# Performance work log

Hardware: AMD Instinct MI355X
Metric: run time of the kernel (lower is better)

## Reference

```python
import jax, jax.numpy as jnp
import numpy as np

N_NODES = 100000
N_HEDGES = 200000
E = 1200000
N_GRAPHS = 512
H = 64            # h_dim
HE = 35           # hedge_fea_dim (CHGConv default)
HOUT = 128        # hout_dim
L = 3             # n_layers
EPS = 1e-5


def _segment_mean(vals, seg, num):
    s = jax.ops.segment_sum(vals, seg, num_segments=num)
    cnt = jax.ops.segment_sum(jnp.ones((vals.shape[0], 1), vals.dtype), seg, num_segments=num)
    return s / jnp.maximum(cnt, 1.0)


def _bn(v, g, b):
    # BatchNorm1d in training mode: batch mean / biased variance
    m = jnp.mean(v, axis=0)
    var = jnp.var(v, axis=0)
    return g * (v - m) * jax.lax.rsqrt(var + EPS) + b


def _chg_conv(x, node_idx, hedge_idx, hattr,
              Wf1, bf1, Wc1, bc1, Wf2, bf2, Wc2, bc2,
              gf, btf, gc, btc, go, bto):
    # gather node feats into hedges, mean-aggregate per hyperedge
    agg = _segment_mean(x[node_idx], hedge_idx, N_HEDGES)          # [NH, H]
    msg = jnp.concatenate([agg, hattr], axis=1)                    # [NH, H+HE]
    z_f = _bn(msg @ Wf1 + bf1, gf, btf)
    z_c = _bn(msg @ Wc1 + bc1, gc, btc)
    hedge_feats = jax.nn.sigmoid(z_f) * jax.nn.softplus(z_c)       # [NH, HE]
    z = jnp.concatenate([x[node_idx], hedge_feats[hedge_idx]], axis=-1)  # [E, H+HE]
    out = jax.nn.sigmoid(z @ Wf2 + bf2) * jax.nn.softplus(z @ Wc2 + bc2)  # [E, H]
    out = _segment_mean(out, node_idx, N_NODES)                    # [N, H]
    out = _bn(out, go, bto)
    return jax.nn.softplus(out + x)


def setup_inputs() -> dict:
    key = jax.random.key(0)
    ks = jax.random.split(key, 32)
    x = jax.random.normal(ks[0], (N_NODES, 92), dtype=jnp.float32)
    node_idx = jax.random.randint(ks[1], (E,), 0, N_NODES)
    hedge_idx = jax.random.randint(ks[2], (E,), 0, N_HEDGES)
    hyperedge_index = jnp.stack([node_idx, hedge_idx], axis=0)     # [2, E]
    hedge_attr = jax.random.normal(ks[3], (N_HEDGES, HE), dtype=jnp.float32)
    batch = jnp.sort(jax.random.randint(ks[4], (N_NODES,), 0, N_GRAPHS))

    s = 0.05
    d = H + HE
    inp = {
        'x': x, 'hyperedge_index': hyperedge_index, 'hedge_attr': hedge_attr, 'batch': batch,
        'We': jax.random.normal(ks[5], (92, H)) * s, 'be': jnp.zeros((H,)),
        'Wf1': jax.random.normal(ks[6], (L, d, HE)) * s, 'bf1': jnp.zeros((L, HE)),
        'Wc1': jax.random.normal(ks[7], (L, d, HE)) * s, 'bc1': jnp.zeros((L, HE)),
        'Wf2': jax.random.normal(ks[8], (L, d, H)) * s, 'bf2': jnp.zeros((L, H)),
        'Wc2': jax.random.normal(ks[9], (L, d, H)) * s, 'bc2': jnp.zeros((L, H)),
        'bn_f_g': jnp.ones((L, HE)), 'bn_f_b': jnp.zeros((L, HE)),
        'bn_c_g': jnp.ones((L, HE)), 'bn_c_b': jnp.zeros((L, HE)),
        'bn_o_g': jnp.ones((L, H)), 'bn_o_b': jnp.zeros((L, H)),
        'Wl2': jax.random.normal(ks[10], (H, HOUT)) * s, 'bl2': jnp.zeros((HOUT,)),
        'Wo': jax.random.normal(ks[11], (HOUT, 1)) * s, 'bo': jnp.zeros((1,)),
    }
    return inp


def reference(x, hyperedge_index, hedge_attr, batch, We, be,
              Wf1, bf1, Wc1, bc1, Wf2, bf2, Wc2, bc2,
              bn_f_g, bn_f_b, bn_c_g, bn_c_b, bn_o_g, bn_o_b,
              Wl2, bl2, Wo, bo):
    node_idx = hyperedge_index[0]
    hedge_idx = hyperedge_index[1]
    h = x @ We + be                                                # embed 92 -> H
    for i in range(L):                                             # only mconvs are used in forward
        h = _chg_conv(h, node_idx, hedge_idx, hedge_attr,
                      Wf1[i], bf1[i], Wc1[i], bc1[i], Wf2[i], bf2[i], Wc2[i], bc2[i],
                      bn_f_g[i], bn_f_b[i], bn_c_g[i], bn_c_b[i], bn_o_g[i], bn_o_b[i])
        h = jax.nn.relu(h)
    g = _segment_mean(h, batch, N_GRAPHS)                          # [G, H]
    g = jax.nn.softplus(g @ Wl2 + bl2)                             # [G, HOUT]
    return g @ Wo + bo                                             # [G, 1]
```

## Files before the change

### kernel.cpp

```cpp
#include <hip/hip_runtime.h>
#include <cstddef>

#define N_NODES_  100000
#define N_HEDGES_ 200000
#define E_        1200000
#define G_        512
#define H_        64
#define HE_       35
#define D_        99
#define HOUT_     128
#define L_        3
#define NBN5_     196
#define NBH5_     391
#define CHUNK_    4096

typedef unsigned int u32;
typedef _Float16 f2_t __attribute__((ext_vector_type(2)));
typedef _Float16 h8_t __attribute__((ext_vector_type(8)));
typedef float f32x4 __attribute__((ext_vector_type(4)));

__device__ __forceinline__ float sigm_(float x){
  return __builtin_amdgcn_rcpf(1.f + __expf(-x));
}
__device__ __forceinline__ float sp_(float x){
  return fmaxf(x, 0.f) + __logf(1.f + __expf(-fabsf(x)));
}
__device__ __forceinline__ float gate_(float F, float C){ return sigm_(F)*sp_(C); }

__device__ __forceinline__ u32 pk_(float a, float b){
  return __builtin_bit_cast(u32, __builtin_amdgcn_cvt_pkrtz(a, b));
}
__device__ __forceinline__ u32 pkadd_(u32 a, u32 b){
  f2_t s = __builtin_bit_cast(f2_t, a) + __builtin_bit_cast(f2_t, b);
  return __builtin_bit_cast(u32, s);
}
__device__ __forceinline__ float dot2_(u32 a, u32 b, float c){
#if __has_builtin(__builtin_amdgcn_fdot2)
  return __builtin_amdgcn_fdot2(__builtin_bit_cast(f2_t, a),
                                __builtin_bit_cast(f2_t, b), c, false);
#else
  f2_t x = __builtin_bit_cast(f2_t, a), y = __builtin_bit_cast(f2_t, b);
  return c + (float)x[0]*(float)y[0] + (float)x[1]*(float)y[1];
#endif
}
__device__ __forceinline__ float lo_(u32 a){ return (float)__builtin_bit_cast(f2_t, a)[0]; }
__device__ __forceinline__ float hi_(u32 a){ return (float)__builtin_bit_cast(f2_t, a)[1]; }

__global__ void k_gcnt(const int* __restrict__ batch, int* __restrict__ gcnt){
  int n = blockIdx.x*256 + threadIdx.x;
  if (n < N_NODES_) atomicAdd(&gcnt[batch[n]], 1);
}
__global__ void k_gscan(const int* __restrict__ gcnt, int* __restrict__ goff){
  __shared__ int tmp[512];
  int t = threadIdx.x;
  int v = gcnt[t];
  tmp[t] = v; __syncthreads();
  for (int d = 1; d < 512; d <<= 1){
    int x = (t >= d) ? tmp[t-d] : 0; __syncthreads();
    tmp[t] += x; __syncthreads();
  }
  goff[t] = tmp[t] - v;
  if (t == 511) goff[512] = tmp[511];
}

__global__ void k_bhist(const int* __restrict__ ni, const int* __restrict__ hi,
                        int* __restrict__ totN, int* __restrict__ totH){
  __shared__ int hN[NBN5_], hH[NBH5_];
  for (int i = threadIdx.x; i < NBN5_; i += 256) hN[i] = 0;
  for (int i = threadIdx.x; i < NBH5_; i += 256) hH[i] = 0;
  __syncthreads();
  int stride = gridDim.x*256;
  for (int e = blockIdx.x*256 + threadIdx.x; e < E_; e += stride){
    atomicAdd(&hN[ni[e] >> 9], 1);
    atomicAdd(&hH[hi[e] >> 9], 1);
  }
  __syncthreads();
  for (int i = threadIdx.x; i < NBN5_; i += 256) if (hN[i]) atomicAdd(&totN[i], hN[i]);
  for (int i = threadIdx.x; i < NBH5_; i += 256) if (hH[i]) atomicAdd(&totH[i], hH[i]);
}

__global__ void k_bscan(const int* __restrict__ totN, const int* __restrict__ totH,
                        int* __restrict__ bbaseN, int* __restrict__ bbaseH,
                        int* __restrict__ gcurN, int* __restrict__ gcurH){
  __shared__ int tmp[512];
  int t = threadIdx.x;
  int v = (t < NBN5_) ? totN[t] : 0;
  tmp[t] = v; __syncthreads();
  for (int d = 1; d < 512; d <<= 1){
    int x = (t >= d) ? tmp[t-d] : 0; __syncthreads();
    tmp[t] += x; __syncthreads();
  }
  if (t < NBN5_){ int b = tmp[t] - v; bbaseN[t] = b; gcurN[t] = b; }
  __syncthreads();
  int w = (t < NBH5_) ? totH[t] : 0;
  tmp[t] = w; __syncthreads();
  for (int d = 1; d < 512; d <<= 1){
    int x = (t >= d) ? tmp[t-d] : 0; __syncthreads();
    tmp[t] += x; __syncthreads();
  }
  if (t < NBH5_){ int b = tmp[t] - w; bbaseH[t] = b; gcurH[t] = b; }
}

__global__ void k_binfill(const int* __restrict__ ni, const int* __restrict__ hi,
                          int* __restrict__ gcurN, int* __restrict__ gcurH,
                          u32* __restrict__ pairN, u32* __restrict__ pairH){
  __shared__ int histN[NBN5_], histH[NBH5_];
  __shared__ int baseN[NBN5_], baseH[NBH5_];
  const int nchunks = (E_ + CHUNK_ - 1)/CHUNK_;
  for (int c = blockIdx.x; c < nchunks; c += gridDim.x){
    int e0 = c*CHUNK_;
    int e1 = e0 + CHUNK_; if (e1 > E_) e1 = E_;
    for (int i = threadIdx.x; i < NBN5_; i += 256) histN[i] = 0;
    for (int i = threadIdx.x; i < NBH5_; i += 256) histH[i] = 0;
    __syncthreads();
    for (int e = e0 + threadIdx.x; e < e1; e += 256){
      atomicAdd(&histN[ni[e] >> 9], 1);
      atomicAdd(&histH[hi[e] >> 9], 1);
    }
    __syncthreads();
    for (int i = threadIdx.x; i < NBN5_; i += 256){
      int hv = histN[i];
      baseN[i] = hv ? atomicAdd(&gcurN[i], hv) : 0;
      histN[i] = 0;
    }
    for (int i = threadIdx.x; i < NBH5_; i += 256){
      int hv = histH[i];
      baseH[i] = hv ? atomicAdd(&gcurH[i], hv) : 0;
      histH[i] = 0;
    }
    __syncthreads();
    for (int e = e0 + threadIdx.x; e < e1; e += 256){
      int n = ni[e], he = hi[e];
      int bn = n >> 9, bh = he >> 9;
      int pn = baseN[bn] + atomicAdd(&histN[bn], 1);
      pairN[pn] = ((u32)(n & 511) << 18) | (u32)he;
      int ph = baseH[bh] + atomicAdd(&histH[bh], 1);
      pairH[ph] = ((u32)(he & 511) << 18) | (u32)n;
    }
    __syncthreads();
  }
}

__global__ void __launch_bounds__(512) k_csrfill2(
    const int* __restrict__ bbase, const int* __restrict__ gcur,
    const u32* __restrict__ pair, int nrows, int* __restrict__ out,
    int* __restrict__ off_arr, int* __restrict__ cnt_arr, float* __restrict__ inv_arr){
  __shared__ int cnt[512], cur[512], tmp[512];
  int b = blockIdx.x, t = threadIdx.x;
  int nb = b*512;
  cnt[t] = 0;
  __syncthreads();
  int base = bbase[b], end = gcur[b];
  for (int pos = base + t; pos < end; pos += 512)
    atomicAdd(&cnt[pair[pos] >> 18], 1);
  __syncthreads();
  int v = cnt[t];
  tmp[t] = v; __syncthreads();
  for (int d = 1; d < 512; d <<= 1){
    int x = (t >= d) ? tmp[t-d] : 0; __syncthreads();
    tmp[t] += x; __syncthreads();
  }
  int ro = base + tmp[t] - v;
  cur[t] = ro;
  int row = nb + t;
  if (row < nrows){
    off_arr[row] = ro;
    cnt_arr[row] = v;
    inv_arr[row] = 1.f/fmaxf((float)v, 1.f);
  }
  __syncthreads();
  for (int pos = base + t; pos < end; pos += 512){
    u32 p = pair[pos];
    int idx = atomicAdd(&cur[p >> 18], 1);
    out[idx] = (int)(p & 0x3FFFFu);
  }
}

__global__ void k_hattr_pack(const float* __restrict__ hattr, u32* __restrict__ hattr16){
  int i = blockIdx.x*256 + threadIdx.x;
  if (i >= N_HEDGES_*18) return;
  int he = i/18, p = i - he*18;
  int k0 = 2*p, k1 = 2*p + 1;
  float w0 = (k0 < 35) ? hattr[(size_t)he*35 + k0] : 0.f;
  float w1 = (k1 < 35) ? hattr[(size_t)he*35 + k1] : 0.f;
  hattr16[i] = pk_(w0, w1);
}

__global__ void k_embed(const float* __restrict__ x, const float* __restrict__ We,
                        const float* __restrict__ be, u32* __restrict__ h16){
  __shared__ __align__(16) float As[64*100];
  __shared__ __align__(16) float Ws[64*100];
  int tid = threadIdx.x;
  for (int idx = tid; idx < 64*100; idx += 256){
    int c = idx/100, k = idx - c*100;
    Ws[idx] = (k < 92) ? We[k*64 + c] : 0.f;
  }
  int rt = tid & 15, ct = tid >> 4;
  float bias[4];
  #pragma unroll
  for (int j = 0; j < 4; ++j) bias[j] = be[ct*4 + j];
  const int ntiles = (N_NODES_ + 63)/64;
  for (int tile = blockIdx.x; tile < ntiles; tile += gridDim.x){
    int rbase = tile*64;
    __syncthreads();
    for (int idx = tid; idx < 64*100; idx += 256){
      int r = idx/100, k = idx - r*100;
      int rg = rbase + r;
      As[idx] = (rg < N_NODES_ && k < 92) ? x[(size_t)rg*92 + k] : 0.f;
    }
    __syncthreads();
    float acc[4][4] = {};
    for (int kc = 0; kc < 25; ++kc){
      float4 av[4], wv[4];
      #pragma unroll
      for (int i = 0; i < 4; ++i) av[i] = *(const float4*)&As[(rt + 16*i)*100 + kc*4];
      #pragma unroll
      for (int j = 0; j < 4; ++j) wv[j] = *(const float4*)&Ws[(ct*4 + j)*100 + kc*4];
      #pragma unroll
      for (int i = 0; i < 4; ++i)
        #pragma unroll
        for (int j = 0; j < 4; ++j)
          acc[i][j] += av[i].x*wv[j].x + av[i].y*wv[j].y + av[i].z*wv[j].z + av[i].w*wv[j].w;
    }
    #pragma unroll
    for (int i = 0; i < 4; ++i){
      int r = rbase + rt + 16*i;
      if (r < N_NODES_){
        h16[(size_t)r*32 + ct*2]     = pk_(acc[i][0] + bias[0], acc[i][1] + bias[1]);
        h16[(size_t)r*32 + ct*2 + 1] = pk_(acc[i][2] + bias[2], acc[i][3] + bias[3]);
      }
    }
  }
}

__global__ void __launch_bounds__(256) k_gather_hedge(
    const u32* __restrict__ h16, const int* __restrict__ hedge_off,
    const int* __restrict__ hcnt, const int* __restrict__ edge_h,
    const float* __restrict__ hinv, u32* __restrict__ hmean16){
  int w = (blockIdx.x*256 + threadIdx.x) >> 3;
  int p = threadIdx.x & 7;
  if (w >= N_HEDGES_) return;
  int off = hedge_off[w], deg = hcnt[w];
  float a[8] = {};
  int i = 0;
  for (; i + 1 < deg; i += 2){
    int n0 = edge_h[off+i], n1 = edge_h[off+i+1];
    uint4 u0 = *(const uint4*)&h16[(size_t)n0*32 + 4*p];
    uint4 u1 = *(const uint4*)&h16[(size_t)n1*32 + 4*p];
    a[0] += lo_(u0.x) + lo_(u1.x); a[1] += hi_(u0.x) + hi_(u1.x);
    a[2] += lo_(u0.y) + lo_(u1.y); a[3] += hi_(u0.y) + hi_(u1.y);
    a[4] += lo_(u0.z) + lo_(u1.z); a[5] += hi_(u0.z) + hi_(u1.z);
    a[6] += lo_(u0.w) + lo_(u1.w); a[7] += hi_(u0.w) + hi_(u1.w);
  }
  if (i < deg){
    uint4 u = *(const uint4*)&h16[(size_t)edge_h[off+i]*32 + 4*p];
    a[0] += lo_(u.x); a[1] += hi_(u.x); a[2] += lo_(u.y); a[3] += hi_(u.y);
    a[4] += lo_(u.z); a[5] += hi_(u.z); a[6] += lo_(u.w); a[7] += hi_(u.w);
  }
  float inv = hinv[w];
  uint4 st;
  st.x = pk_(a[0]*inv, a[1]*inv); st.y = pk_(a[2]*inv, a[3]*inv);
  st.z = pk_(a[4]*inv, a[5]*inv); st.w = pk_(a[6]*inv, a[7]*inv);
  *(uint4*)&hmean16[(size_t)w*32 + 4*p] = st;
}

__global__ void k_hedge_mlp1(const u32* __restrict__ hmean16, const u32* __restrict__ hattr16,
                             const float* __restrict__ Wf1, const float* __restrict__ bf1,
                             const float* __restrict__ Wc1, const float* __restrict__ bc1,
                             __fp16* __restrict__ tfc16T, float* __restrict__ hstats){
  __shared__ __align__(16) u32 As16[64*68];
  __shared__ __align__(16) u32 Ws16[80*68];
  __shared__ float sstat[160];
  int tid = threadIdx.x;
  for (int idx = tid; idx < 80*68; idx += 256){
    int c = idx/68, kk = idx - c*68;
    int k0 = 2*kk, k1 = k0 + 1;
    float w0 = 0.f, w1 = 0.f;
    if (c < 70){
      int cc = (c < 35) ? c : c - 35;
      const float* W = (c < 35) ? Wf1 : Wc1;
      if (k0 < 99) w0 = W[k0*35 + cc];
      if (k1 < 99) w1 = W[k1*35 + cc];
    }
    Ws16[idx] = pk_(w0, w1);
  }
  for (int idx = tid; idx < 160; idx += 256) sstat[idx] = 0.f;
  int lane = tid & 63, wv = tid >> 6;
  int l15 = lane & 15, lg = lane >> 4;
  float bias[5];
  #pragma unroll
  for (int t = 0; t < 5; ++t){
    int c = t*16 + l15;
    bias[t] = (c < 35) ? bf1[c] : (c < 70 ? bc1[c - 35] : 0.f);
  }
  float sreg[5] = {}, qreg[5] = {};
  for (int tile = blockIdx.x; tile < N_HEDGES_/64; tile += gridDim.x){
    int rbase = tile*64;
    __syncthreads();
    for (int idx = tid; idx < 64*68; idx += 256){
      int r = idx/68, kk = idx - r*68;
      int rg = rbase + r;
      u32 v = 0;
      if (kk < 32)      v = hmean16[(size_t)rg*32 + kk];
      else if (kk < 50) v = hattr16[(size_t)rg*18 + (kk - 32)];
      As16[idx] = v;
    }
    __syncthreads();
    h8_t af[4];
    int arow = wv*16 + l15;
    #pragma unroll
    for (int ks = 0; ks < 4; ++ks)
      af[ks] = *(const h8_t*)&As16[arow*68 + ks*16 + lg*4];
    __syncthreads();
    __fp16* Cs = (__fp16*)As16;
    f32x4 acc[5];
    #pragma unroll
    for (int t = 0; t < 5; ++t) acc[t] = (f32x4){0.f,0.f,0.f,0.f};
    #pragma unroll
    for (int t = 0; t < 5; ++t){
      int bcol = t*16 + l15;
      #pragma unroll
      for (int ks = 0; ks < 4; ++ks){
        h8_t bf = *(const h8_t*)&Ws16[bcol*68 + ks*16 + lg*4];
        acc[t] = __builtin_amdgcn_mfma_f32_16x16x32_f16(af[ks], bf, acc[t], 0, 0, 0);
      }
    }
    #pragma unroll
    for (int t = 0; t < 5; ++t){
      int col = t*16 + l15;
      #pragma unroll
      for (int q = 0; q < 4; ++q){
        float v = acc[t][q] + bias[t];
        int row = wv*16 + lg*4 + q;
        Cs[col*72 + row] = (__fp16)v;
        sreg[t] += v; qreg[t] += v*v;
      }
    }
    __syncthreads();
    for (int idx = tid; idx < 70*8; idx += 256){
      int col = idx >> 3, seg = idx & 7;
      uint4 v = *(const uint4*)&Cs[col*72 + seg*8];
      *(uint4*)&tfc16T[(size_t)col*N_HEDGES_ + rbase + seg*8] = v;
    }
  }
  #pragma unroll
  for (int t = 0; t < 5; ++t){
    float s = sreg[t], q = qreg[t];
    s += __shfl_xor(s, 16); q += __shfl_xor(q, 16);
    s += __shfl_xor(s, 32); q += __shfl_xor(q, 32);
    if (lg == 0){
      int c = t*16 + l15;
      if (c < 70){
        atomicAdd(&sstat[c], s);
        atomicAdd(&sstat[80 + c], q);
      }
    }
  }
  __syncthreads();
  for (int idx = tid; idx < 160; idx += 256) atomicAdd(&hstats[idx], sstat[idx]);
}

__global__ void k_bn_fin_hedge(const float* __restrict__ stats,
                               const float* __restrict__ gf, const float* __restrict__ btf,
                               const float* __restrict__ gc, const float* __restrict__ btc,
                               float* __restrict__ ab, float invN){
  int j = threadIdx.x;
  if (j >= 70) return;
  float m = stats[j]*invN;
  float var = stats[80+j]*invN - m*m;
  float gg = (j < 35) ? gf[j] : gc[j-35];
  float bb = (j < 35) ? btf[j] : btc[j-35];
  float a = gg*rsqrtf(var + 1e-5f);
  ab[j] = a; ab[70+j] = bb - m*a;
}

__global__ void k_hedge_feats(const __fp16* __restrict__ tfc16T, const float* __restrict__ ab,
                              const float* __restrict__ Wf2, const float* __restrict__ bf2,
                              const float* __restrict__ Wc2, const float* __restrict__ bc2,
                              u32* __restrict__ heFC2){
  __shared__ __align__(16) u32 As16[64*20];
  __shared__ __align__(16) u32 Ws16[128*20];
  int tid = threadIdx.x;
  for (int idx = tid; idx < 128*20; idx += 256){
    int c = idx/20, kk = idx - c*20;
    int k0 = 2*kk, k1 = 2*kk + 1;
    float w0 = 0.f, w1 = 0.f;
    if (k0 < 35) w0 = (c < 64) ? Wf2[(64+k0)*64 + c] : Wc2[(64+k0)*64 + (c-64)];
    if (k1 < 35) w1 = (c < 64) ? Wf2[(64+k1)*64 + c] : Wc2[(64+k1)*64 + (c-64)];
    Ws16[idx] = pk_(w0, w1);
  }
  int rt = tid & 15, ct = tid >> 4;
  float biasF[4], biasC[4];
  #pragma unroll
  for (int j = 0; j < 4; ++j){ biasF[j] = bf2[ct*4 + j]; biasC[j] = bc2[ct*4 + j]; }
  for (int tile = blockIdx.x; tile < N_HEDGES_/64; tile += gridDim.x){
    int rbase = tile*64;
    __syncthreads();
    for (int idx = tid; idx < 64*20; idx += 256){
      int kk = idx >> 6;
      int r  = idx & 63;
      float a0 = 0.f, a1 = 0.f;
      if (kk < 18){
        int rg = rbase + r;
        int k0 = 2*kk, k1 = 2*kk + 1;
        {
          float tf = (float)tfc16T[(size_t)k0*N_HEDGES_ + rg];
          float tc = (float)tfc16T[(size_t)(35+k0)*N_HEDGES_ + rg];
          float zf = ab[k0]*tf + ab[70 + k0];
          float zc = ab[35+k0]*tc + ab[105 + k0];
          a0 = gate_(zf, zc);
        }
        if (k1 < 35){
          float tf = (float)tfc16T[(size_t)k1*N_HEDGES_ + rg];
          float tc = (float)tfc16T[(size_t)(35+k1)*N_HEDGES_ + rg];
          float zf = ab[k1]*tf + ab[70 + k1];
          float zc = ab[35+k1]*tc + ab[105 + k1];
          a1 = gate_(zf, zc);
        }
      }
      As16[r*20 + kk] = pk_(a0, a1);
    }
    __syncthreads();
    float accF[4][4] = {}, accC[4][4] = {};
    for (int kc = 0; kc < 5; ++kc){
      uint4 av[4], wF[4], wC[4];
      #pragma unroll
      for (int i = 0; i < 4; ++i) av[i] = *(const uint4*)&As16[(rt + 16*i)*20 + kc*4];
      #pragma unroll
      for (int j = 0; j < 4; ++j){
        wF[j] = *(const uint4*)&Ws16[(ct*4 + j)*20 + kc*4];
        wC[j] = *(const uint4*)&Ws16[(64 + ct*4 + j)*20 + kc*4];
      }
      #pragma unroll
      for (int i = 0; i < 4; ++i)
        #pragma unroll
        for (int j = 0; j < 4; ++j){
          float f = accF[i][j], c = accC[i][j];
          f = dot2_(av[i].x, wF[j].x, f); c = dot2_(av[i].x, wC[j].x, c);
          f = dot2_(av[i].y, wF[j].y, f); c = dot2_(av[i].y, wC[j].y, c);
          f = dot2_(av[i].z, wF[j].z, f); c = dot2_(av[i].z, wC[j].z, c);
          f = dot2_(av[i].w, wF[j].w, f); c = dot2_(av[i].w, wC[j].w, c);
          accF[i][j] = f; accC[i][j] = c;
        }
    }
    #pragma unroll
    for (int i = 0; i < 4; ++i){
      int r = rbase + rt + 16*i;
      #pragma unroll
      for (int j = 0; j < 4; ++j){
        heFC2[(size_t)r*64 + ct*4 + j] = pk_(accF[i][j] + biasF[j], accC[i][j] + biasC[j]);
      }
    }
  }
}

__global__ void k_node_lin(const u32* __restrict__ h16,
                           const float* __restrict__ Wf2, const float* __restrict__ Wc2,
                           u32* __restrict__ nFC2){
  __shared__ __align__(16) u32 As16[64*36];
  __shared__ __align__(16) u32 Ws16[128*36];
  int tid = threadIdx.x;
  for (int idx = tid; idx < 128*36; idx += 256){
    int c = idx/36, kk = idx - c*36;
    int k0 = 2*kk, k1 = 2*kk + 1;
    float w0 = 0.f, w1 = 0.f;
    if (k0 < 64) w0 = (c < 64) ? Wf2[k0*64 + c] : Wc2[k0*64 + (c-64)];
    if (k1 < 64) w1 = (c < 64) ? Wf2[k1*64 + c] : Wc2[k1*64 + (c-64)];
    Ws16[idx] = pk_(w0, w1);
  }
  int rt = tid & 15, ct = tid >> 4;
  const int ntiles = (N_NODES_ + 63)/64;
  for (int tile = blockIdx.x; tile < ntiles; tile += gridDim.x){
    int rbase = tile*64;
    __syncthreads();
    for (int idx = tid; idx < 64*36; idx += 256){
      int r = idx/36, kk = idx - r*36;
      int rg = rbase + r;
      As16[idx] = (rg < N_NODES_ && kk < 32) ? h16[(size_t)rg*32 + kk] : 0u;
    }
    __syncthreads();
    float accF[4][4] = {}, accC[4][4] = {};
    for (int kc = 0; kc < 8; ++kc){
      uint4 av[4], wF[4], wC[4];
      #pragma unroll
      for (int i = 0; i < 4; ++i) av[i] = *(const uint4*)&As16[(rt + 16*i)*36 + kc*4];
      #pragma unroll
      for (int j = 0; j < 4; ++j){
        wF[j] = *(const uint4*)&Ws16[(ct*4 + j)*36 + kc*4];
        wC[j] = *(const uint4*)&Ws16[(64 + ct*4 + j)*36 + kc*4];
      }
      #pragma unroll
      for (int i = 0; i < 4; ++i)
        #pragma unroll
        for (int j = 0; j < 4; ++j){
          float f = accF[i][j], c = accC[i][j];
          f = dot2_(av[i].x, wF[j].x, f); c = dot2_(av[i].x, wC[j].x, c);
          f = dot2_(av[i].y, wF[j].y, f); c = dot2_(av[i].y, wC[j].y, c);
          f = dot2_(av[i].z, wF[j].z, f); c = dot2_(av[i].z, wC[j].z, c);
          f = dot2_(av[i].w, wF[j].w, f); c = dot2_(av[i].w, wC[j].w, c);
          accF[i][j] = f; accC[i][j] = c;
        }
    }
    #pragma unroll
    for (int i = 0; i < 4; ++i){
      int r = rbase + rt + 16*i;
      if (r < N_NODES_){
        #pragma unroll
        for (int j = 0; j < 4; ++j){
          nFC2[(size_t)r*64 + ct*4 + j] = pk_(accF[i][j], accC[i][j]);
        }
      }
    }
  }
}

__global__ void k_edge(const u32* __restrict__ nFC2, const u32* __restrict__ heFC2,
                       const int* __restrict__ node_off, const int* __restrict__ ndeg,
                       const int* __restrict__ edge_n, const float* __restrict__ ninv,
                       __fp16* __restrict__ nmean16, float* __restrict__ nstats){
  int lane = threadIdx.x & 63, wave = threadIdx.x >> 6;
  float s = 0.f, q = 0.f;
  for (int base = blockIdx.x*4; base < N_NODES_; base += gridDim.x*4){
    int n = base + wave;
    if (n < N_NODES_){
      int off = __builtin_amdgcn_readfirstlane(node_off[n]);
      int deg = __builtin_amdgcn_readfirstlane(ndeg[n]);
      u32 p0 = nFC2[(size_t)n*64 + lane];
      float acc = 0.f;
      int i = 0;
      for (; i + 7 < deg; i += 8){
        int e0 = edge_n[off+i],   e1 = edge_n[off+i+1], e2 = edge_n[off+i+2], e3 = edge_n[off+i+3];
        int e4 = edge_n[off+i+4], e5 = edge_n[off+i+5], e6 = edge_n[off+i+6], e7 = edge_n[off+i+7];
        u32 s0 = pkadd_(p0, heFC2[(size_t)e0*64 + lane]);
        u32 s1 = pkadd_(p0, heFC2[(size_t)e1*64 + lane]);
        u32 s2 = pkadd_(p0, heFC2[(size_t)e2*64 + lane]);
        u32 s3 = pkadd_(p0, heFC2[(size_t)e3*64 + lane]);
        u32 s4 = pkadd_(p0, heFC2[(size_t)e4*64 + lane]);
        u32 s5 = pkadd_(p0, heFC2[(size_t)e5*64 + lane]);
        u32 s6 = pkadd_(p0, heFC2[(size_t)e6*64 + lane]);
        u32 s7 = pkadd_(p0, heFC2[(size_t)e7*64 + lane]);
        acc += gate_(lo_(s0), hi_(s0)) + gate_(lo_(s1), hi_(s1))
             + gate_(lo_(s2), hi_(s2)) + gate_(lo_(s3), hi_(s3))
             + gate_(lo_(s4), hi_(s4)) + gate_(lo_(s5), hi_(s5))
             + gate_(lo_(s6), hi_(s6)) + gate_(lo_(s7), hi_(s7));
      }
      for (; i + 3 < deg; i += 4){
        int e0 = edge_n[off+i], e1 = edge_n[off+i+1], e2 = edge_n[off+i+2], e3 = edge_n[off+i+3];
        u32 s0 = pkadd_(p0, heFC2[(size_t)e0*64 + lane]);
        u32 s1 = pkadd_(p0, heFC2[(size_t)e1*64 + lane]);
        u32 s2 = pkadd_(p0, heFC2[(size_t)e2*64 + lane]);
        u32 s3 = pkadd_(p0, heFC2[(size_t)e3*64 + lane]);
        acc += gate_(lo_(s0), hi_(s0)) + gate_(lo_(s1), hi_(s1))
             + gate_(lo_(s2), hi_(s2)) + gate_(lo_(s3), hi_(s3));
      }
      for (; i < deg; ++i){
        u32 sA = pkadd_(p0, heFC2[(size_t)edge_n[off+i]*64 + lane]);
        acc += gate_(lo_(sA), hi_(sA));
      }
      float m = acc * ninv[n];
      nmean16[(size_t)n*64 + lane] = (__fp16)m;
      s += m; q += m*m;
    }
  }
  __shared__ float p1[256], p2[256];
  p1[threadIdx.x] = s; p2[threadIdx.x] = q;
  __syncthreads();
  if (wave == 0){
    float a = p1[lane] + p1[64+lane] + p1[128+lane] + p1[192+lane];
    float b = p2[lane] + p2[64+lane] + p2[128+lane] + p2[192+lane];
    atomicAdd(&nstats[lane], a);
    atomicAdd(&nstats[64+lane], b);
  }
}

__global__ void k_bn_fin_node(const float* __restrict__ stats, const float* __restrict__ g,
                              const float* __restrict__ bt, float* __restrict__ ab, float invN){
  int j = threadIdx.x;
  if (j >= 64) return;
  float m = stats[j]*invN;
  float var = stats[64+j]*invN - m*m;
  float a = g[j]*rsqrtf(var + 1e-5f);
  ab[j] = a; ab[64+j] = bt[j] - m*a;
}

__global__ void k_node_update(const u32* __restrict__ nmean16, const float* __restrict__ ab,
                              const u32* __restrict__ h16, u32* __restrict__ h16out){
  int t = blockIdx.x*256 + threadIdx.x;
  if (t >= N_NODES_*32) return;
  int p = t & 31;
  int f0 = 2*p, f1 = 2*p + 1;
  u32 nm = nmean16[t];
  u32 hh = h16[t];
  float r0 = sp_(ab[f0]*lo_(nm) + ab[64+f0] + lo_(hh));
  float r1 = sp_(ab[f1]*hi_(nm) + ab[64+f1] + hi_(hh));
  h16out[t] = pk_(r0, r1);
}

__global__ void __launch_bounds__(256) k_graph_agg2(
    const u32* __restrict__ h16, const int* __restrict__ goff,
    float* __restrict__ gmean){
  __shared__ float s0[256], s1[256];
  int g = blockIdx.x;
  int st = goff[g], en = goff[g+1];
  int p = threadIdx.x & 31;
  int r = threadIdx.x >> 5;
  float a0 = 0.f, a1 = 0.f;
  for (int n = st + r; n < en; n += 8){
    u32 u = h16[(size_t)n*32 + p];
    a0 += lo_(u); a1 += hi_(u);
  }
  s0[threadIdx.x] = a0; s1[threadIdx.x] = a1;
  __syncthreads();
  for (int d = 128; d >= 32; d >>= 1){
    if (threadIdx.x < d){
      s0[threadIdx.x] += s0[threadIdx.x + d];
      s1[threadIdx.x] += s1[threadIdx.x + d];
    }
    __syncthreads();
  }
  if (threadIdx.x < 32){
    float inv = 1.f/fmaxf((float)(en - st), 1.f);
    gmean[(size_t)g*64 + 2*threadIdx.x]     = s0[threadIdx.x]*inv;
    gmean[(size_t)g*64 + 2*threadIdx.x + 1] = s1[threadIdx.x]*inv;
  }
}

__global__ void k_head(const float* __restrict__ gmean,
                       const float* __restrict__ Wl2, const float* __restrict__ bl2,
                       const float* __restrict__ Wo, const float* __restrict__ bo,
                       float* __restrict__ out){
  __shared__ float gm[64];
  __shared__ float red[128];
  int g = blockIdx.x, j = threadIdx.x;
  if (j < 64) gm[j] = gmean[(size_t)g*64+j];
  __syncthreads();
  float u = bl2[j];
  for (int f = 0; f < 64; ++f) u += gm[f]*Wl2[f*128+j];
  red[j] = sp_(u)*Wo[j];
  __syncthreads();
  for (int s = 64; s > 0; s >>= 1){
    if (j < s) red[j] += red[j+s];
    __syncthreads();
  }
  if (j == 0) out[g] = red[0] + bo[0];
}

extern "C" void kernel_launch(void* const* d_in, const int* in_sizes, int n_in,
                              void* d_out, int out_size, void* d_ws, size_t ws_size,
                              hipStream_t stream){
  (void)in_sizes; (void)n_in; (void)out_size; (void)ws_size;
  const float* x      = (const float*)d_in[0];
  const int*   ni     = (const int*)d_in[1];
  const int*   hi     = ni + E_;
  const float* hattr  = (const float*)d_in[2];
  const int*   batch  = (const int*)d_in[3];
  const float* We     = (const float*)d_in[4];
  const float* be     = (const float*)d_in[5];
  const float* Wf1    = (const float*)d_in[6];
  const float* bf1    = (const float*)d_in[7];
  const float* Wc1    = (const float*)d_in[8];
  const float* bc1    = (const float*)d_in[9];
  const float* Wf2    = (const float*)d_in[10];
  const float* bf2    = (const float*)d_in[11];
  const float* Wc2    = (const float*)d_in[12];
  const float* bc2    = (const float*)d_in[13];
  const float* bn_f_g = (const float*)d_in[14];
  const float* bn_f_b = (const float*)d_in[15];
  const float* bn_c_g = (const float*)d_in[16];
  const float* bn_c_b = (const float*)d_in[17];
  const float* bn_o_g = (const float*)d_in[18];
  const float* bn_o_b = (const float*)d_in[19];
  const float* Wl2    = (const float*)d_in[20];
  const float* bl2    = (const float*)d_in[21];
  const float* Wo     = (const float*)d_in[22];
  const float* bo     = (const float*)d_in[23];

  float* ws = (float*)d_ws;
  size_t o = 0;
  __fp16* tfc16T = (__fp16*)(ws + o); o += (size_t)N_HEDGES_*70/2 + 64;
  u32*   nFC2  = (u32*)tfc16T;
  u32*   pairN = (u32*)tfc16T;
  u32*   pairH = pairN + E_;
  float* hmR   = ws + o; o += (size_t)N_HEDGES_*H_;
  u32*   hmean16 = (u32*)hmR;
  u32*   heFC2   = (u32*)hmR;
  __fp16* nmean16 = (__fp16*)(ws + o); o += (size_t)N_NODES_*H_/2 + 64;
  u32*  h16a   = (u32*)(ws + o); o += (size_t)N_NODES_*32;
  u32*  h16b   = (u32*)(ws + o); o += (size_t)N_NODES_*32;
  u32*  hattr16= (u32*)(ws + o); o += (size_t)N_HEDGES_*18;
  float* hstats = ws + o; o += 256;
  float* habs   = ws + o; o += 256;
  float* nstats = ws + o; o += 128;
  float* nabs   = ws + o; o += 128;
  float* gmean  = ws + o; o += (size_t)G_*H_;
  float* hinv   = ws + o; o += N_HEDGES_;
  float* ninv   = ws + o; o += N_NODES_;
  int* hcnt     = (int*)(ws + o); o += N_HEDGES_;
  int* ndeg     = (int*)(ws + o); o += N_NODES_;
  int* gcnt     = (int*)(ws + o); o += G_;
  int* goff     = (int*)(ws + o); o += G_ + 1;
  int* node_off = (int*)(ws + o); o += N_NODES_;
  int* hedge_off= (int*)(ws + o); o += N_HEDGES_;
  int* gcurN    = (int*)(ws + o); o += NBN5_;
  int* gcurH    = (int*)(ws + o); o += NBH5_;
  int* totN     = (int*)(ws + o); o += NBN5_;
  int* totH     = (int*)(ws + o); o += NBH5_;
  int* bbaseN   = (int*)(ws + o); o += NBN5_;
  int* bbaseH   = (int*)(ws + o); o += NBH5_;
  int* edge_n   = (int*)(ws + o); o += E_;
  int* edge_h   = (int*)(ws + o); o += E_;

  hipMemsetAsync(totN, 0, sizeof(int)*(NBN5_ + NBH5_), stream);
  hipMemsetAsync(gcnt, 0, sizeof(int)*G_, stream);

  k_gcnt<<<(N_NODES_+255)/256, 256, 0, stream>>>(batch, gcnt);
  k_gscan<<<1, 512, 0, stream>>>(gcnt, goff);
  k_hattr_pack<<<(N_HEDGES_*18+255)/256, 256, 0, stream>>>(hattr, hattr16);

  k_bhist<<<512, 256, 0, stream>>>(ni, hi, totN, totH);
  k_bscan<<<1, 512, 0, stream>>>(totN, totH, bbaseN, bbaseH, gcurN, gcurH);
  k_binfill<<<(E_+CHUNK_-1)/CHUNK_, 256, 0, stream>>>(ni, hi, gcurN, gcurH, pairN, pairH);
  k_csrfill2<<<NBN5_, 512, 0, stream>>>(bbaseN, gcurN, pairN, N_NODES_, edge_n,
                                        node_off, ndeg, ninv);
  k_csrfill2<<<NBH5_, 512, 0, stream>>>(bbaseH, gcurH, pairH, N_HEDGES_, edge_h,
                                        hedge_off, hcnt, hinv);

  k_embed<<<768, 256, 0, stream>>>(x, We, be, h16a);

  u32* hc16 = h16a;
  u32* hn16 = h16b;
  for (int l = 0; l < L_; ++l){
    const float* Wf1l = Wf1 + (size_t)l*D_*HE_;
    const float* Wc1l = Wc1 + (size_t)l*D_*HE_;
    const float* Wf2l = Wf2 + (size_t)l*D_*H_;
    const float* Wc2l = Wc2 + (size_t)l*D_*H_;

    hipMemsetAsync(hstats, 0, sizeof(float)*160, stream);
    hipMemsetAsync(nstats, 0, sizeof(float)*128, stream);

    k_gather_hedge<<<(N_HEDGES_*8+255)/256, 256, 0, stream>>>(hc16, hedge_off, hcnt, edge_h,
                                                              hinv, hmean16);
    k_hedge_mlp1<<<1280, 256, 0, stream>>>(hmean16, hattr16, Wf1l, bf1 + l*HE_,
                                           Wc1l, bc1 + l*HE_, tfc16T, hstats);
    k_bn_fin_hedge<<<1, 128, 0, stream>>>(hstats, bn_f_g + l*HE_, bn_f_b + l*HE_,
                                          bn_c_g + l*HE_, bn_c_b + l*HE_, habs,
                                          1.f/(float)N_HEDGES_);
    k_hedge_feats<<<1536, 256, 0, stream>>>(tfc16T, habs, Wf2l, bf2 + l*H_,
                                            Wc2l, bc2 + l*H_, heFC2);
    k_node_lin<<<1024, 256, 0, stream>>>(hc16, Wf2l, Wc2l, nFC2);
    k_edge<<<2048, 256, 0, stream>>>(nFC2, heFC2, node_off, ndeg, edge_n, ninv,
                                     nmean16, nstats);
    k_bn_fin_node<<<1, 64, 0, stream>>>(nstats, bn_o_g + l*H_, bn_o_b + l*H_, nabs,
                                        1.f/(float)N_NODES_);
    k_node_update<<<(N_NODES_*32+255)/256, 256, 0, stream>>>((const u32*)nmean16, nabs,
                                                             hc16, hn16);
    u32* t3 = hc16; hc16 = hn16; hn16 = t3;
  }

  k_graph_agg2<<<G_, 256, 0, stream>>>(hc16, goff, gmean);
  k_head<<<G_, 128, 0, stream>>>(gmean, Wl2, bl2, Wo, bo, (float*)d_out);
}
```

Baseline: 1.161 ms.

## Load MFMA A-fragments directly from global and use MFMA in node linear

The hedge MLP1 kernel now loads A-operand fragments straight from global memory into registers instead of staging them through shared memory, and writes its transposed outputs directly rather than through a shared-memory transpose buffer. This removes several block barriers per tile. The node linear kernel replaces its scalar dot2 FMA loop with 16x16x32 f16 MFMA instructions, also loading A directly from global. The trade-off is less coalesced global stores (8-byte scattered writes to the transposed layout) in exchange for fewer syncs and matrix-core throughput.

```diff
diff --git a/kernel.cpp b/kernel.cpp
--- a/kernel.cpp
+++ b/kernel.cpp
@@ -264,11 +264,11 @@
   *(uint4*)&hmean16[(size_t)w*32 + 4*p] = st;
 }
 
-__global__ void k_hedge_mlp1(const u32* __restrict__ hmean16, const u32* __restrict__ hattr16,
-                             const float* __restrict__ Wf1, const float* __restrict__ bf1,
-                             const float* __restrict__ Wc1, const float* __restrict__ bc1,
-                             __fp16* __restrict__ tfc16T, float* __restrict__ hstats){
-  __shared__ __align__(16) u32 As16[64*68];
+__global__ void __launch_bounds__(256) k_hedge_mlp1(
+    const u32* __restrict__ hmean16, const u32* __restrict__ hattr16,
+    const float* __restrict__ Wf1, const float* __restrict__ bf1,
+    const float* __restrict__ Wc1, const float* __restrict__ bc1,
+    __fp16* __restrict__ tfc16T, float* __restrict__ hstats){
   __shared__ __align__(16) u32 Ws16[80*68];
   __shared__ float sstat[160];
   int tid = threadIdx.x;
@@ -285,6 +285,7 @@
     Ws16[idx] = pk_(w0, w1);
   }
   for (int idx = tid; idx < 160; idx += 256) sstat[idx] = 0.f;
+  __syncthreads();
   int lane = tid & 63, wv = tid >> 6;
   int l15 = lane & 15, lg = lane >> 4;
   float bias[5];
@@ -296,51 +297,45 @@
   float sreg[5] = {}, qreg[5] = {};
   for (int tile = blockIdx.x; tile < N_HEDGES_/64; tile += gridDim.x){
     int rbase = tile*64;
-    __syncthreads();
-    for (int idx = tid; idx < 64*68; idx += 256){
-      int r = idx/68, kk = idx - r*68;
-      int rg = rbase + r;
-      u32 v = 0;
-      if (kk < 32)      v = hmean16[(size_t)rg*32 + kk];
-      else if (kk < 50) v = hattr16[(size_t)rg*18 + (kk - 32)];
-      As16[idx] = v;
-    }
-    __syncthreads();
-    h8_t af[4];
-    int arow = wv*16 + l15;
-    #pragma unroll
-    for (int ks = 0; ks < 4; ++ks)
-      af[ks] = *(const h8_t*)&As16[arow*68 + ks*16 + lg*4];
-    __syncthreads();
-    __fp16* Cs = (__fp16*)As16;
+    int arow = rbase + wv*16 + l15;
+    h8_t af0 = *(const h8_t*)&hmean16[(size_t)arow*32 + lg*4];
+    h8_t af1 = *(const h8_t*)&hmean16[(size_t)arow*32 + 16 + lg*4];
+    uint2 b0 = *(const uint2*)&hattr16[(size_t)arow*18 + lg*4];
+    uint2 b1 = *(const uint2*)&hattr16[(size_t)arow*18 + lg*4 + 2];
+    uint4 a2; a2.x = b0.x; a2.y = b0.y; a2.z = b1.x; a2.w = b1.y;
+    h8_t af2 = __builtin_bit_cast(h8_t, a2);
+    uint4 a3 = {0u,0u,0u,0u};
+    if (lg == 0){
+      uint2 u = *(const uint2*)&hattr16[(size_t)arow*18 + 16];
+      a3.x = u.x; a3.y = u.y;
+    }
+    h8_t af3 = __builtin_bit_cast(h8_t, a3);
     f32x4 acc[5];
     #pragma unroll
     for (int t = 0; t < 5; ++t) acc[t] = (f32x4){0.f,0.f,0.f,0.f};
     #pragma unroll
     for (int t = 0; t < 5; ++t){
       int bcol = t*16 + l15;
-      #pragma unroll
-      for (int ks = 0; ks < 4; ++ks){
-        h8_t bf = *(const h8_t*)&Ws16[bcol*68 + ks*16 + lg*4];
-        acc[t] = __builtin_amdgcn_mfma_f32_16x16x32_f16(af[ks], bf, acc[t], 0, 0, 0);
-      }
+      h8_t bf0 = *(const h8_t*)&Ws16[bcol*68 + 0*16 + lg*4];
+      h8_t bf1_ = *(const h8_t*)&Ws16[bcol*68 + 1*16 + lg*4];
+      h8_t bf2_ = *(const h8_t*)&Ws16[bcol*68 + 2*16 + lg*4];
+      h8_t bf3_ = *(const h8_t*)&Ws16[bcol*68 + 3*16 + lg*4];
+      acc[t] = __builtin_amdgcn_mfma_f32_16x16x32_f16(af0, bf0, acc[t], 0, 0, 0);
+      acc[t] = __builtin_amdgcn_mfma_f32_16x16x32_f16(af1, bf1_, acc[t], 0, 0, 0);
+      acc[t] = __builtin_amdgcn_mfma_f32_16x16x32_f16(af2, bf2_, acc[t], 0, 0, 0);
+      acc[t] = __builtin_amdgcn_mfma_f32_16x16x32_f16(af3, bf3_, acc[t], 0, 0, 0);
     }
     #pragma unroll
     for (int t = 0; t < 5; ++t){
       int col = t*16 + l15;
-      #pragma unroll
-      for (int q = 0; q < 4; ++q){
-        float v = acc[t][q] + bias[t];
-        int row = wv*16 + lg*4 + q;
-        Cs[col*72 + row] = (__fp16)v;
-        sreg[t] += v; qreg[t] += v*v;
-      }
-    }
-    __syncthreads();
-    for (int idx = tid; idx < 70*8; idx += 256){
-      int col = idx >> 3, seg = idx & 7;
-      uint4 v = *(const uint4*)&Cs[col*72 + seg*8];
-      *(uint4*)&tfc16T[(size_t)col*N_HEDGES_ + rbase + seg*8] = v;
+      float v0 = acc[t][0] + bias[t], v1 = acc[t][1] + bias[t];
+      float v2 = acc[t][2] + bias[t], v3 = acc[t][3] + bias[t];
+      sreg[t] += v0 + v1 + v2 + v3;
+      qreg[t] += v0*v0 + v1*v1 + v2*v2 + v3*v3;
+      if (col < 70){
+        uint2 st; st.x = pk_(v0, v1); st.y = pk_(v2, v3);
+        *(uint2*)&tfc16T[(size_t)col*N_HEDGES_ + rbase + wv*16 + lg*4] = st;
+      }
     }
   }
   #pragma unroll
@@ -454,61 +449,54 @@
   }
 }
 
-__global__ void k_node_lin(const u32* __restrict__ h16,
-                           const float* __restrict__ Wf2, const float* __restrict__ Wc2,
-                           u32* __restrict__ nFC2){
-  __shared__ __align__(16) u32 As16[64*36];
+__global__ void __launch_bounds__(256) k_node_lin(
+    const u32* __restrict__ h16,
+    const float* __restrict__ Wf2, const float* __restrict__ Wc2,
+    u32* __restrict__ nFC2){
   __shared__ __align__(16) u32 Ws16[128*36];
   int tid = threadIdx.x;
   for (int idx = tid; idx < 128*36; idx += 256){
     int c = idx/36, kk = idx - c*36;
-    int k0 = 2*kk, k1 = 2*kk + 1;
+    int k0 = 2*kk, k1 = k0 + 1;
     float w0 = 0.f, w1 = 0.f;
     if (k0 < 64) w0 = (c < 64) ? Wf2[k0*64 + c] : Wc2[k0*64 + (c-64)];
     if (k1 < 64) w1 = (c < 64) ? Wf2[k1*64 + c] : Wc2[k1*64 + (c-64)];
     Ws16[idx] = pk_(w0, w1);
   }
-  int rt = tid & 15, ct = tid >> 4;
+  __syncthreads();
+  int lane = tid & 63, wv = tid >> 6;
+  int l15 = lane & 15, lg = lane >> 4;
   const int ntiles = (N_NODES_ + 63)/64;
   for (int tile = blockIdx.x; tile < ntiles; tile += gridDim.x){
     int rbase = tile*64;
-    __syncthreads();
-    for (int idx = tid; idx < 64*36; idx += 256){
-      int r = idx/36, kk = idx - r*36;
-      int rg = rbase + r;
-      As16[idx] = (rg < N_NODES_ && kk < 32) ? h16[(size_t)rg*32 + kk] : 0u;
-    }
-    __syncthreads();
-    float accF[4][4] = {}, accC[4][4] = {};
-    for (int kc = 0; kc < 8; ++kc){
-      uint4 av[4], wF[4], wC[4];
+    int arow = rbase + wv*16 + l15;
+    h8_t af0, af1;
+    if (arow < N_NODES_){
+      af0 = *(const h8_t*)&h16[(size_t)arow*32 + lg*4];
+      af1 = *(const h8_t*)&h16[(size_t)arow*32 + 16 + lg*4];
+    } else {
+      uint4 z = {0u,0u,0u,0u};
+      af0 = __builtin_bit_cast(h8_t, z);
+      af1 = __builtin_bit_cast(h8_t, z);
+    }
+    f32x4 acc[8];
+    #pragma unroll
+    for (int t = 0; t < 8; ++t) acc[t] = (f32x4){0.f,0.f,0.f,0.f};
+    #pragma unroll
+    for (int t = 0; t < 8; ++t){
+      int bcol = t*16 + l15;
+      h8_t bf0 = *(const h8_t*)&Ws16[bcol*36 + 0*16 + lg*4];
+      h8_t bf1 = *(const h8_t*)&Ws16[bcol*36 + 1*16 + lg*4];
+      acc[t] = __builtin_amdgcn_mfma_f32_16x16x32_f16(af0, bf0, acc[t], 0, 0, 0);
+      acc[t] = __builtin_amdgcn_mfma_f32_16x16x32_f16(af1, bf1, acc[t], 0, 0, 0);
+    }
+    #pragma unroll
+    for (int t = 0; t < 4; ++t){
       #pragma unroll
-      for (int i = 0; i < 4; ++i) av[i] = *(const uint4*)&As16[(rt + 16*i)*36 + kc*4];
-      #pragma unroll
-      for (int j = 0; j < 4; ++j){
-        wF[j] = *(const uint4*)&Ws16[(ct*4 + j)*36 + kc*4];
-        wC[j] = *(const uint4*)&Ws16[(64 + ct*4 + j)*36 + kc*4];
-      }
-      #pragma unroll
-      for (int i = 0; i < 4; ++i)
-        #pragma unroll
-        for (int j = 0; j < 4; ++j){
-          float f = accF[i][j], c = accC[i][j];
-          f = dot2_(av[i].x, wF[j].x, f); c = dot2_(av[i].x, wC[j].x, c);
-          f = dot2_(av[i].y, wF[j].y, f); c = dot2_(av[i].y, wC[j].y, c);
-          f = dot2_(av[i].z, wF[j].z, f); c = dot2_(av[i].z, wC[j].z, c);
-          f = dot2_(av[i].w, wF[j].w, f); c = dot2_(av[i].w, wC[j].w, c);
-          accF[i][j] = f; accC[i][j] = c;
-        }
-    }
-    #pragma unroll
-    for (int i = 0; i < 4; ++i){
-      int r = rbase + rt + 16*i;
-      if (r < N_NODES_){
-        #pragma unroll
-        for (int j = 0; j < 4; ++j){
-          nFC2[(size_t)r*64 + ct*4 + j] = pk_(accF[i][j], accC[i][j]);
-        }
+      for (int q = 0; q < 4; ++q){
+        int row = rbase + wv*16 + lg*4 + q;
+        if (row < N_NODES_)
+          nFC2[(size_t)row*64 + t*16 + l15] = pk_(acc[t][q], acc[t+4][q]);
       }
     }
   }
```

Measured after the change: 1.017 ms. 12.4% less time.
